# Performance work log

Hardware: AMD Instinct MI355X
Metric: run time of the kernel (lower is better)

## Reference

```python
import jax, jax.numpy as jnp
import numpy as np

NUM_HEADS = 32
NUM_KV_HEADS = 8
HEAD_DIM = 128
WINDOW = 512
NUM_META = 4


def _swa_sink_mask(S):
    # allowed = causal & (within sliding window OR sink/meta token)
    i = jnp.arange(S)[:, None]   # q_idx
    j = jnp.arange(S)[None, :]   # kv_idx
    return (i >= j) & (((i - j) <= WINDOW) | (j < NUM_META))


def setup_inputs() -> dict:
    key = jax.random.key(0)
    k1, k2, k3 = jax.random.split(key, 3)
    B, S = 1, 2048
    return {
        "query_states": jax.random.normal(k1, (B, S, NUM_HEADS * HEAD_DIM), dtype=jnp.float32),
        "key_states": jax.random.normal(k2, (B, S, NUM_KV_HEADS * HEAD_DIM), dtype=jnp.float32),
        "value_states": jax.random.normal(k3, (B, S, NUM_KV_HEADS * HEAD_DIM), dtype=jnp.float32),
    }


def reference(query_states, key_states, value_states):
    B, S, _ = query_states.shape
    n_rep = NUM_HEADS // NUM_KV_HEADS
    # [B, H, S, D]
    q = query_states.reshape(B, S, NUM_HEADS, HEAD_DIM).transpose(0, 2, 1, 3)
    k = key_states.reshape(B, S, NUM_KV_HEADS, HEAD_DIM).transpose(0, 2, 1, 3)
    v = value_states.reshape(B, S, NUM_KV_HEADS, HEAD_DIM).transpose(0, 2, 1, 3)
    # repeat_kv: interleaved repeat along head dim (GQA)
    k = jnp.repeat(k, n_rep, axis=1)
    v = jnp.repeat(v, n_rep, axis=1)

    scale = 1.0 / jnp.sqrt(jnp.float32(HEAD_DIM))  # flex_attention default scale
    scores = jnp.einsum("bhqd,bhkd->bhqk", q, k) * scale
    mask = _swa_sink_mask(S)  # [S, S], every row has q_idx==kv_idx allowed
    scores = jnp.where(mask[None, None], scores, -jnp.inf)
    attn = jax.nn.softmax(scores, axis=-1)
    out = jnp.einsum("bhqk,bhkd->bhqd", attn, v)
    return out.transpose(0, 2, 1, 3).reshape(B, S, NUM_HEADS * HEAD_DIM)
```

## Files before the change

### kernel.cpp

```cpp
#include <hip/hip_runtime.h>
#include <math.h>

typedef __attribute__((ext_vector_type(8))) short bf16x8;
typedef __attribute__((ext_vector_type(16))) float f32x16;

#define NH 32
#define DIMH 128
#define WIN 512
#define META 4
#define TQ 128
#define TK 64
#define KSTR 132
#define VSTR 68
#define PSTRD 34
#define QSCALE 0.08838834764831845f
#define MFIX 14.0f

union U8 { int4 i4; bf16x8 bf; };

__device__ __forceinline__ unsigned bf16_rne(float x) {
  unsigned u = __float_as_uint(x);
  return (u + 0x7FFFu + ((u >> 16) & 1u)) >> 16;
}
__device__ __forceinline__ unsigned pk2(float a, float b) {
  return bf16_rne(a) | (bf16_rne(b) << 16);
}

__global__ void cvt_k(const float* __restrict__ K, unsigned short* __restrict__ Kb) {
  int i = (blockIdx.x * 256 + threadIdx.x) * 4;
  float4 v = *(const float4*)(K + i);
  *(uint2*)(Kb + i) = make_uint2(pk2(v.x, v.y), pk2(v.z, v.w));
}

__global__ __launch_bounds__(256) void cvt_v(const float* __restrict__ V,
                                             unsigned short* __restrict__ Vt) {
  __shared__ float tile[64 * 33];
  const int p = blockIdx.x, hk = blockIdx.y, dt = blockIdx.z;
  const int t = threadIdx.x;
  #pragma unroll
  for (int it = 0; it < 2; ++it) {
    int u = it * 256 + t;
    int key = u >> 3, c = u & 7;
    float4 v = *(const float4*)(V + (size_t)(p * 64 + key) * 1024 + hk * DIMH + dt * 32 + c * 4);
    float* dst = &tile[key * 33 + c * 4];
    dst[0] = v.x; dst[1] = v.y; dst[2] = v.z; dst[3] = v.w;
  }
  __syncthreads();
  const int dim = t >> 3, s0 = (t & 7) * 8;
  float f[8];
  #pragma unroll
  for (int s = 0; s < 8; ++s) {
    int sl = s0 + s;
    int key = (sl >> 1) + 32 * (sl & 1);
    f[s] = tile[key * 33 + dim];
  }
  int4 out = make_int4(pk2(f[0], f[1]), pk2(f[2], f[3]), pk2(f[4], f[5]), pk2(f[6], f[7]));
  *(int4*)(Vt + ((size_t)((hk * 32 + p) * 128 + dt * 32 + dim)) * 64 + s0) = out;
}

__global__ __launch_bounds__(256, 2) void swa_mfma(
    const float* __restrict__ Qg, const unsigned short* __restrict__ Kb,
    const unsigned short* __restrict__ Vt, float* __restrict__ Og)
{
  __shared__ __align__(16) char smem[34304];
  __shared__ __align__(16) unsigned Pw[4 * 32 * PSTRD];
  unsigned short* Ks  = (unsigned short*)smem;
  unsigned short* Vts = (unsigned short*)(smem + 16896);
  unsigned short* Qs  = (unsigned short*)smem;

  const int tid = threadIdx.x;
  const int q0 = blockIdx.x * TQ;
  const int h = blockIdx.y, hk = h >> 2;
  const int lane = tid & 63, wid = tid >> 6;
  const int cl = lane & 31, hl = lane >> 5;

  #pragma unroll
  for (int it = 0; it < 16; ++it) {
    int u = it * 256 + tid;
    int row = u >> 5, d4 = (u & 31) * 4;
    float4 v = *(const float4*)(Qg + (size_t)(q0 + row) * 4096 + h * DIMH + d4);
    *(uint2*)(Qs + row * KSTR + d4) =
        make_uint2(pk2(v.x * QSCALE, v.y * QSCALE), pk2(v.z * QSCALE, v.w * QSCALE));
  }
  __syncthreads();
  int4 qf[8];
  {
    const int row = wid * 32 + cl;
    #pragma unroll
    for (int kc = 0; kc < 8; ++kc) {
      const unsigned short* src = Qs + row * KSTR + kc * 16 + hl * 8;
      uint2 lo = *(const uint2*)src;
      uint2 hi = *(const uint2*)(src + 4);
      qf[kc] = make_int4(lo.x, lo.y, hi.x, hi.y);
    }
  }
  __syncthreads();

  f32x16 acc[4];
  #pragma unroll
  for (int nt = 0; nt < 4; ++nt)
    #pragma unroll
    for (int i = 0; i < 16; ++i) acc[nt][i] = 0.f;
  float lp[16];
  #pragma unroll
  for (int i = 0; i < 16; ++i) lp[i] = 0.f;

  unsigned* PwW = Pw + wid * 32 * PSTRD;

  const int jstart = (q0 > WIN) ? (q0 - WIN) : 0;
  const int sink = (jstart > 0) ? 1 : 0;
  const int niter = (q0 - jstart + TQ) / TK + sink;

  for (int t = 0; t < niter; ++t) {
    const int jt = (sink && t == 0) ? 0 : jstart + (t - sink) * TK;
    const bool needMask = (jt + 63 > q0) || (q0 + 127 - jt > WIN);

    __syncthreads();
    #pragma unroll
    for (int it = 0; it < 4; ++it) {
      int u = it * 256 + tid;
      int key = u >> 4, s16 = (u & 15) * 8;
      int4 d = *(const int4*)(Kb + (size_t)(jt + key) * 1024 + hk * DIMH + s16);
      *(int4*)(Ks + key * KSTR + s16) = d;
    }
    {
      const size_t vbase = (size_t)(hk * 32 + (jt >> 6)) * 128 * 64;
      #pragma unroll
      for (int it = 0; it < 4; ++it) {
        int u = it * 256 + tid;
        int dim = u >> 3, s8 = (u & 7) * 8;
        int4 d = *(const int4*)(Vt + vbase + (size_t)dim * 64 + s8);
        *(int4*)(Vts + dim * VSTR + s8) = d;
      }
    }
    __syncthreads();

    f32x16 s0v, s1v;
    #pragma unroll
    for (int i = 0; i < 16; ++i) { s0v[i] = 0.f; s1v[i] = 0.f; }
    #pragma unroll
    for (int kc = 0; kc < 8; ++kc) {
      U8 a; a.i4 = qf[kc];
      const unsigned short* k0p = Ks + cl * KSTR + kc * 16 + hl * 8;
      U8 b0; { uint2 lo = *(const uint2*)k0p; uint2 hi = *(const uint2*)(k0p + 4);
               b0.i4 = make_int4(lo.x, lo.y, hi.x, hi.y); }
      s0v = __builtin_amdgcn_mfma_f32_32x32x16_bf16(a.bf, b0.bf, s0v, 0, 0, 0);
      const unsigned short* k1p = k0p + 32 * KSTR;
      U8 b1; { uint2 lo = *(const uint2*)k1p; uint2 hi = *(const uint2*)(k1p + 4);
               b1.i4 = make_int4(lo.x, lo.y, hi.x, hi.y); }
      s1v = __builtin_amdgcn_mfma_f32_32x32x16_bf16(a.bf, b1.bf, s1v, 0, 0, 0);
    }

    const int k0 = jt + cl, k1 = jt + 32 + cl;
    #pragma unroll
    for (int ri = 0; ri < 16; ++ri) {
      const int rl = (ri & 3) + 8 * (ri >> 2) + 4 * hl;
      float s0 = s0v[ri] - MFIX;
      float s1 = s1v[ri] - MFIX;
      if (needMask) {
        const int row = q0 + wid * 32 + rl;
        const int d0 = row - k0, d1 = row - k1;
        if (!((d0 >= 0) && ((d0 <= WIN) || (k0 < META)))) s0 = -1e30f;
        if (!((d1 >= 0) && ((d1 <= WIN) || (k1 < META)))) s1 = -1e30f;
      }
      float p0 = __expf(s0), p1 = __expf(s1);
      unsigned u0 = __float_as_uint(p0) & 0xFFFF0000u;
      unsigned u1 = __float_as_uint(p1) & 0xFFFF0000u;
      lp[ri] += __uint_as_float(u0) + __uint_as_float(u1);
      PwW[rl * PSTRD + cl] = (u0 >> 16) | u1;
    }
    __syncthreads();

    #pragma unroll
    for (int kc = 0; kc < 4; ++kc) {
      const unsigned* ap = PwW + cl * PSTRD + kc * 8 + hl * 4;
      U8 a; { uint2 lo = *(const uint2*)ap; uint2 hi = *(const uint2*)(ap + 2);
              a.i4 = make_int4(lo.x, lo.y, hi.x, hi.y); }
      #pragma unroll
      for (int nt = 0; nt < 4; ++nt) {
        const unsigned short* vp = Vts + (nt * 32 + cl) * VSTR + kc * 16 + hl * 8;
        U8 b; { uint2 lo = *(const uint2*)vp; uint2 hi = *(const uint2*)(vp + 4);
                b.i4 = make_int4(lo.x, lo.y, hi.x, hi.y); }
        acc[nt] = __builtin_amdgcn_mfma_f32_32x32x16_bf16(a.bf, b.bf, acc[nt], 0, 0, 0);
      }
    }
  }

  #pragma unroll
  for (int ri = 0; ri < 16; ++ri) {
    float v = lp[ri];
    v += __shfl_xor(v, 1);  v += __shfl_xor(v, 2);  v += __shfl_xor(v, 4);
    v += __shfl_xor(v, 8);  v += __shfl_xor(v, 16);
    lp[ri] = __fdividef(1.0f, v);
  }
  #pragma unroll
  for (int nt = 0; nt < 4; ++nt) {
    #pragma unroll
    for (int ri = 0; ri < 16; ++ri) {
      const int rl = (ri & 3) + 8 * (ri >> 2) + 4 * hl;
      Og[(size_t)(q0 + wid * 32 + rl) * 4096 + h * DIMH + nt * 32 + cl] = acc[nt][ri] * lp[ri];
    }
  }
}

extern "C" void kernel_launch(void* const* d_in, const int* in_sizes, int n_in,
                              void* d_out, int out_size, void* d_ws, size_t ws_size,
                              hipStream_t stream) {
  const float* Q = (const float*)d_in[0];
  const float* K = (const float*)d_in[1];
  const float* V = (const float*)d_in[2];
  float* O = (float*)d_out;
  unsigned short* Kb = (unsigned short*)d_ws;
  unsigned short* Vt = Kb + (size_t)2048 * 1024;

  hipLaunchKernelGGL(cvt_k, dim3(2048), dim3(256), 0, stream, K, Kb);
  hipLaunchKernelGGL(cvt_v, dim3(32, 8, 4), dim3(256), 0, stream, V, Vt);
  hipLaunchKernelGGL(swa_mfma, dim3(2048 / TQ, NH), dim3(256), 0, stream, Q, Kb, Vt, O);
}
```

Measured before the change: 136.7 us.

## Drop shared-memory K/V staging, load MFMA operands directly from global per wave

The attention kernel no longer stages K and V tiles in LDS with block-wide barriers. Each wave now reads its bf16 K and transposed V fragments straight from global memory (relying on cache) and prefetches V fragments one step ahead, and it works on its own 32-row query range with tighter per-wave key bounds. The sink tile issues only the first V chunk's MFMAs. Q is converted directly into registers, and the two conversion pre-kernels are merged into one launch. This removes barriers and LDS traffic but adds redundant global and L2 reads across waves.

```diff
diff --git a/kernel.cpp b/kernel.cpp
--- a/kernel.cpp
+++ b/kernel.cpp
@@ -5,13 +5,8 @@
 typedef __attribute__((ext_vector_type(16))) float f32x16;
 
 #define NH 32
-#define DIMH 128
 #define WIN 512
 #define META 4
-#define TQ 128
-#define TK 64
-#define KSTR 132
-#define VSTR 68
 #define PSTRD 34
 #define QSCALE 0.08838834764831845f
 #define MFIX 14.0f
@@ -26,22 +21,27 @@
   return bf16_rne(a) | (bf16_rne(b) << 16);
 }
 
-__global__ void cvt_k(const float* __restrict__ K, unsigned short* __restrict__ Kb) {
-  int i = (blockIdx.x * 256 + threadIdx.x) * 4;
-  float4 v = *(const float4*)(K + i);
-  *(uint2*)(Kb + i) = make_uint2(pk2(v.x, v.y), pk2(v.z, v.w));
-}
-
-__global__ __launch_bounds__(256) void cvt_v(const float* __restrict__ V,
-                                             unsigned short* __restrict__ Vt) {
+__global__ __launch_bounds__(256) void prepass(
+    const float* __restrict__ K, const float* __restrict__ V,
+    unsigned short* __restrict__ Kb, unsigned short* __restrict__ Vt)
+{
   __shared__ float tile[64 * 33];
-  const int p = blockIdx.x, hk = blockIdx.y, dt = blockIdx.z;
-  const int t = threadIdx.x;
+  const int b = blockIdx.x, t = threadIdx.x;
+
+  {
+    const size_t i = ((size_t)b * 256 + t) * 8;
+    float4 x = *(const float4*)(K + i);
+    float4 y = *(const float4*)(K + i + 4);
+    *(int4*)(Kb + i) = make_int4(pk2(x.x, x.y), pk2(x.z, x.w),
+                                 pk2(y.x, y.y), pk2(y.z, y.w));
+  }
+
+  const int hk = b >> 7, rem = b & 127, p = rem >> 2, dt = rem & 3;
   #pragma unroll
   for (int it = 0; it < 2; ++it) {
     int u = it * 256 + t;
     int key = u >> 3, c = u & 7;
-    float4 v = *(const float4*)(V + (size_t)(p * 64 + key) * 1024 + hk * DIMH + dt * 32 + c * 4);
+    float4 v = *(const float4*)(V + (size_t)(p * 64 + key) * 1024 + hk * 128 + dt * 32 + c * 4);
     float* dst = &tile[key * 33 + c * 4];
     dst[0] = v.x; dst[1] = v.y; dst[2] = v.z; dst[3] = v.w;
   }
@@ -54,47 +54,33 @@
     int key = (sl >> 1) + 32 * (sl & 1);
     f[s] = tile[key * 33 + dim];
   }
-  int4 out = make_int4(pk2(f[0], f[1]), pk2(f[2], f[3]), pk2(f[4], f[5]), pk2(f[6], f[7]));
-  *(int4*)(Vt + ((size_t)((hk * 32 + p) * 128 + dt * 32 + dim)) * 64 + s0) = out;
-}
-
-__global__ __launch_bounds__(256, 2) void swa_mfma(
+  *(int4*)(Vt + ((size_t)((hk * 32 + p) * 128 + dt * 32 + dim)) * 64 + s0) =
+      make_int4(pk2(f[0], f[1]), pk2(f[2], f[3]), pk2(f[4], f[5]), pk2(f[6], f[7]));
+}
+
+__global__ __launch_bounds__(256, 2) void swa_main(
     const float* __restrict__ Qg, const unsigned short* __restrict__ Kb,
     const unsigned short* __restrict__ Vt, float* __restrict__ Og)
 {
-  __shared__ __align__(16) char smem[34304];
   __shared__ __align__(16) unsigned Pw[4 * 32 * PSTRD];
-  unsigned short* Ks  = (unsigned short*)smem;
-  unsigned short* Vts = (unsigned short*)(smem + 16896);
-  unsigned short* Qs  = (unsigned short*)smem;
 
   const int tid = threadIdx.x;
-  const int q0 = blockIdx.x * TQ;
-  const int h = blockIdx.y, hk = h >> 2;
   const int lane = tid & 63, wid = tid >> 6;
   const int cl = lane & 31, hl = lane >> 5;
-
-  #pragma unroll
-  for (int it = 0; it < 16; ++it) {
-    int u = it * 256 + tid;
-    int row = u >> 5, d4 = (u & 31) * 4;
-    float4 v = *(const float4*)(Qg + (size_t)(q0 + row) * 4096 + h * DIMH + d4);
-    *(uint2*)(Qs + row * KSTR + d4) =
-        make_uint2(pk2(v.x * QSCALE, v.y * QSCALE), pk2(v.z * QSCALE, v.w * QSCALE));
-  }
-  __syncthreads();
+  const int h = blockIdx.y, hk = h >> 2;
+  const int q0 = (blockIdx.x * 4 + wid) * 32;
+
   int4 qf[8];
   {
-    const int row = wid * 32 + cl;
+    const float* qrow = Qg + (size_t)(q0 + cl) * 4096 + h * 128 + hl * 8;
     #pragma unroll
     for (int kc = 0; kc < 8; ++kc) {
-      const unsigned short* src = Qs + row * KSTR + kc * 16 + hl * 8;
-      uint2 lo = *(const uint2*)src;
-      uint2 hi = *(const uint2*)(src + 4);
-      qf[kc] = make_int4(lo.x, lo.y, hi.x, hi.y);
-    }
-  }
-  __syncthreads();
+      float4 x = *(const float4*)(qrow + kc * 16);
+      float4 y = *(const float4*)(qrow + kc * 16 + 4);
+      qf[kc] = make_int4(pk2(x.x*QSCALE, x.y*QSCALE), pk2(x.z*QSCALE, x.w*QSCALE),
+                         pk2(y.x*QSCALE, y.y*QSCALE), pk2(y.z*QSCALE, y.w*QSCALE));
+    }
+  }
 
   f32x16 acc[4];
   #pragma unroll
@@ -107,81 +93,79 @@
 
   unsigned* PwW = Pw + wid * 32 * PSTRD;
 
-  const int jstart = (q0 > WIN) ? (q0 - WIN) : 0;
+  const int jstart = (q0 > WIN) ? ((q0 - WIN) & ~63) : 0;
   const int sink = (jstart > 0) ? 1 : 0;
-  const int niter = (q0 - jstart + TQ) / TK + sink;
+  const int niter = ((q0 + 31 - jstart) >> 6) + 1 + sink;
 
   for (int t = 0; t < niter; ++t) {
-    const int jt = (sink && t == 0) ? 0 : jstart + (t - sink) * TK;
-    const bool needMask = (jt + 63 > q0) || (q0 + 127 - jt > WIN);
-
-    __syncthreads();
-    #pragma unroll
-    for (int it = 0; it < 4; ++it) {
-      int u = it * 256 + tid;
-      int key = u >> 4, s16 = (u & 15) * 8;
-      int4 d = *(const int4*)(Kb + (size_t)(jt + key) * 1024 + hk * DIMH + s16);
-      *(int4*)(Ks + key * KSTR + s16) = d;
-    }
-    {
-      const size_t vbase = (size_t)(hk * 32 + (jt >> 6)) * 128 * 64;
-      #pragma unroll
-      for (int it = 0; it < 4; ++it) {
-        int u = it * 256 + tid;
-        int dim = u >> 3, s8 = (u & 7) * 8;
-        int4 d = *(const int4*)(Vt + vbase + (size_t)dim * 64 + s8);
-        *(int4*)(Vts + dim * VSTR + s8) = d;
-      }
-    }
-    __syncthreads();
-
+    const bool isSink = (sink != 0) && (t == 0);
+    const int jt = isSink ? 0 : jstart + ((t - sink) << 6);
+    const bool needMask = (jt + 63 > q0) || (q0 + 31 - jt > WIN);
+
+    const unsigned short* kb0 = Kb + (size_t)(jt + cl) * 1024 + hk * 128 + hl * 8;
     f32x16 s0v, s1v;
     #pragma unroll
     for (int i = 0; i < 16; ++i) { s0v[i] = 0.f; s1v[i] = 0.f; }
     #pragma unroll
     for (int kc = 0; kc < 8; ++kc) {
       U8 a; a.i4 = qf[kc];
-      const unsigned short* k0p = Ks + cl * KSTR + kc * 16 + hl * 8;
-      U8 b0; { uint2 lo = *(const uint2*)k0p; uint2 hi = *(const uint2*)(k0p + 4);
-               b0.i4 = make_int4(lo.x, lo.y, hi.x, hi.y); }
+      U8 b0; b0.i4 = *(const int4*)(kb0 + kc * 16);
       s0v = __builtin_amdgcn_mfma_f32_32x32x16_bf16(a.bf, b0.bf, s0v, 0, 0, 0);
-      const unsigned short* k1p = k0p + 32 * KSTR;
-      U8 b1; { uint2 lo = *(const uint2*)k1p; uint2 hi = *(const uint2*)(k1p + 4);
-               b1.i4 = make_int4(lo.x, lo.y, hi.x, hi.y); }
+      U8 b1; b1.i4 = *(const int4*)(kb0 + 32 * 1024 + kc * 16);
       s1v = __builtin_amdgcn_mfma_f32_32x32x16_bf16(a.bf, b1.bf, s1v, 0, 0, 0);
     }
+
+    const unsigned short* vb = Vt + (size_t)((hk * 32 + (jt >> 6)) * 128) * 64 + cl * 64 + hl * 8;
+    U8 vcur[4];
+    #pragma unroll
+    for (int nt = 0; nt < 4; ++nt)
+      vcur[nt].i4 = *(const int4*)(vb + nt * 2048);
 
     const int k0 = jt + cl, k1 = jt + 32 + cl;
     #pragma unroll
     for (int ri = 0; ri < 16; ++ri) {
       const int rl = (ri & 3) + 8 * (ri >> 2) + 4 * hl;
-      float s0 = s0v[ri] - MFIX;
-      float s1 = s1v[ri] - MFIX;
+      float sa = s0v[ri] - MFIX;
+      float sb = s1v[ri] - MFIX;
       if (needMask) {
-        const int row = q0 + wid * 32 + rl;
+        const int row = q0 + rl;
         const int d0 = row - k0, d1 = row - k1;
-        if (!((d0 >= 0) && ((d0 <= WIN) || (k0 < META)))) s0 = -1e30f;
-        if (!((d1 >= 0) && ((d1 <= WIN) || (k1 < META)))) s1 = -1e30f;
+        if (!((d0 >= 0) && ((d0 <= WIN) || (k0 < META)))) sa = -1e30f;
+        if (!((d1 >= 0) && ((d1 <= WIN) || (k1 < META)))) sb = -1e30f;
       }
-      float p0 = __expf(s0), p1 = __expf(s1);
+      float p0 = __expf(sa), p1 = __expf(sb);
       unsigned u0 = __float_as_uint(p0) & 0xFFFF0000u;
       unsigned u1 = __float_as_uint(p1) & 0xFFFF0000u;
       lp[ri] += __uint_as_float(u0) + __uint_as_float(u1);
       PwW[rl * PSTRD + cl] = (u0 >> 16) | u1;
     }
-    __syncthreads();
-
-    #pragma unroll
-    for (int kc = 0; kc < 4; ++kc) {
-      const unsigned* ap = PwW + cl * PSTRD + kc * 8 + hl * 4;
+
+    if (isSink) {
+      const unsigned* ap = PwW + cl * PSTRD + hl * 4;
       U8 a; { uint2 lo = *(const uint2*)ap; uint2 hi = *(const uint2*)(ap + 2);
               a.i4 = make_int4(lo.x, lo.y, hi.x, hi.y); }
       #pragma unroll
-      for (int nt = 0; nt < 4; ++nt) {
-        const unsigned short* vp = Vts + (nt * 32 + cl) * VSTR + kc * 16 + hl * 8;
-        U8 b; { uint2 lo = *(const uint2*)vp; uint2 hi = *(const uint2*)(vp + 4);
-                b.i4 = make_int4(lo.x, lo.y, hi.x, hi.y); }
-        acc[nt] = __builtin_amdgcn_mfma_f32_32x32x16_bf16(a.bf, b.bf, acc[nt], 0, 0, 0);
+      for (int nt = 0; nt < 4; ++nt)
+        acc[nt] = __builtin_amdgcn_mfma_f32_32x32x16_bf16(a.bf, vcur[nt].bf, acc[nt], 0, 0, 0);
+    } else {
+      #pragma unroll
+      for (int kc = 0; kc < 4; ++kc) {
+        U8 vnext[4];
+        if (kc < 3) {
+          #pragma unroll
+          for (int nt = 0; nt < 4; ++nt)
+            vnext[nt].i4 = *(const int4*)(vb + nt * 2048 + (kc + 1) * 16);
+        }
+        const unsigned* ap = PwW + cl * PSTRD + kc * 8 + hl * 4;
+        U8 a; { uint2 lo = *(const uint2*)ap; uint2 hi = *(const uint2*)(ap + 2);
+                a.i4 = make_int4(lo.x, lo.y, hi.x, hi.y); }
+        #pragma unroll
+        for (int nt = 0; nt < 4; ++nt)
+          acc[nt] = __builtin_amdgcn_mfma_f32_32x32x16_bf16(a.bf, vcur[nt].bf, acc[nt], 0, 0, 0);
+        if (kc < 3) {
+          #pragma unroll
+          for (int nt = 0; nt < 4; ++nt) vcur[nt] = vnext[nt];
+        }
       }
     }
   }
@@ -198,7 +182,7 @@
     #pragma unroll
     for (int ri = 0; ri < 16; ++ri) {
       const int rl = (ri & 3) + 8 * (ri >> 2) + 4 * hl;
-      Og[(size_t)(q0 + wid * 32 + rl) * 4096 + h * DIMH + nt * 32 + cl] = acc[nt][ri] * lp[ri];
+      Og[(size_t)(q0 + rl) * 4096 + h * 128 + nt * 32 + cl] = acc[nt][ri] * lp[ri];
     }
   }
 }
@@ -213,7 +197,6 @@
   unsigned short* Kb = (unsigned short*)d_ws;
   unsigned short* Vt = Kb + (size_t)2048 * 1024;
 
-  hipLaunchKernelGGL(cvt_k, dim3(2048), dim3(256), 0, stream, K, Kb);
-  hipLaunchKernelGGL(cvt_v, dim3(32, 8, 4), dim3(256), 0, stream, V, Vt);
-  hipLaunchKernelGGL(swa_mfma, dim3(2048 / TQ, NH), dim3(256), 0, stream, Q, Kb, Vt, O);
-}
+  hipLaunchKernelGGL(prepass, dim3(1024), dim3(256), 0, stream, K, V, Kb, Vt);
+  hipLaunchKernelGGL(swa_main, dim3(16, NH), dim3(256), 0, stream, Q, Kb, Vt, O);
+}
```

Result: slower. 167.4 us (+22.4%).
